# Optimization experiments

Measured on AMD Instinct MI355X. Metric: run time of the kernel, lower is better.

Reference implementation:

```python
import jax, jax.numpy as jnp
import numpy as np

H, KVH, D = 32, 8, 128            # query heads, kv heads, head dim
HIDDEN = H * D                     # 4096
B, S = 32, 2048                    # decode batch, max kv length
THETA = 10000.0
SCALE = D ** -0.5


def setup_inputs() -> dict:
    key = jax.random.key(0)
    ks = jax.random.split(key, 6)
    return {
        "hidden_states": jax.random.normal(ks[0], (B, HIDDEN), jnp.float32),
        "w_qkv": jax.random.normal(ks[1], ((H + 2 * KVH) * D, HIDDEN), jnp.float32) * (HIDDEN ** -0.5),
        "w_o": jax.random.normal(ks[2], (HIDDEN, HIDDEN), jnp.float32) * (HIDDEN ** -0.5),
        "k_cache": jax.random.normal(ks[3], (B, S, KVH, D), jnp.float32),
        "v_cache": jax.random.normal(ks[4], (B, S, KVH, D), jnp.float32),
        "positions": jax.random.randint(ks[5], (B,), 0, S, jnp.int32),
    }


def _rope(x, positions):
    # x: [B, nheads, D], neox-style rotary over full head dim
    half = D // 2
    inv_freq = 1.0 / (THETA ** (jnp.arange(0, half, dtype=jnp.float32) / half))
    freqs = positions.astype(jnp.float32)[:, None] * inv_freq[None, :]   # [B, half]
    cos = jnp.cos(freqs)[:, None, :]
    sin = jnp.sin(freqs)[:, None, :]
    x1, x2 = x[..., :half], x[..., half:]
    return jnp.concatenate([x1 * cos - x2 * sin, x2 * cos + x1 * sin], axis=-1)


def reference(hidden_states, w_qkv, w_o, k_cache, v_cache, positions):
    G = H // KVH  # query heads per kv head
    qkv = hidden_states @ w_qkv.T                      # [B, (H+2*KVH)*D]
    q, k, v = jnp.split(qkv, [H * D, (H + KVH) * D], axis=-1)
    q = _rope(q.reshape(B, H, D), positions)           # [B, H, D]
    k = _rope(k.reshape(B, KVH, D), positions)         # [B, KVH, D]
    v = v.reshape(B, KVH, D)

    # write current token's k/v into the cache at its position (paged-cache write)
    slot = (jnp.arange(S)[None, :] == positions[:, None])[:, :, None, None]  # [B,S,1,1]
    keys = jnp.where(slot, k[:, None], k_cache)        # [B, S, KVH, D]
    vals = jnp.where(slot, v[:, None], v_cache)

    qg = q.reshape(B, KVH, G, D)
    scores = jnp.einsum("bkgd,bskd->bkgs", qg, keys) * SCALE   # [B, KVH, G, S]
    valid = (jnp.arange(S)[None, :] <= positions[:, None])[:, None, None, :]
    scores = jnp.where(valid, scores, -jnp.inf)
    probs = jax.nn.softmax(scores, axis=-1)
    attn = jnp.einsum("bkgs,bskd->bkgd", probs, vals).reshape(B, H * D)
    return attn @ w_o.T                                # [B, HIDDEN]
```

## Files before the change

### kernel.cpp

```cpp
#include <hip/hip_runtime.h>
#include <hip/hip_bf16.h>

#define NH   32
#define NKVH 8
#define NG   4
#define DD   128
#define HID  4096
#define NQKV 6144
#define NB   32
#define SS   2048
#define SCALE 0.08838834764831845f
#define CHUNK 256
#define NCHUNK 8

typedef __attribute__((ext_vector_type(4))) float f32x4;
typedef __attribute__((ext_vector_type(8))) short bf16x8;

static __device__ __forceinline__ unsigned short f2bf(float f) {
    __hip_bfloat16 h = __float2bfloat16(f);
    return __builtin_bit_cast(unsigned short, h);
}

__global__ void cvt_hs(const float* __restrict__ in, unsigned short* __restrict__ out) {
    int i = blockIdx.x * 256 + threadIdx.x;
    out[i] = f2bf(in[i]);
}

__global__ __launch_bounds__(256) void gemm32(
    const unsigned short* __restrict__ Abf,
    const float* __restrict__ W,
    float* __restrict__ Out,
    int K, int N) {
    int j0 = blockIdx.x * 16;
    int tid = threadIdx.x;
    int wave = tid >> 6;
    int lane = tid & 63;
    int l16 = lane & 15;
    int kgrp = lane >> 4;
    int Kq = K >> 2;
    int kbeg = wave * Kq, kend = kbeg + Kq;

    f32x4 acc0 = {0.f, 0.f, 0.f, 0.f};
    f32x4 acc1 = {0.f, 0.f, 0.f, 0.f};
    const unsigned short* arow0 = Abf + (size_t)l16 * K;
    const unsigned short* arow1 = Abf + (size_t)(16 + l16) * K;
    const float* wrow = W + (size_t)(j0 + l16) * K;

#pragma unroll 2
    for (int k = kbeg; k < kend; k += 32) {
        int kk = k + kgrp * 8;
        bf16x8 a0 = *(const bf16x8*)(arow0 + kk);
        bf16x8 a1 = *(const bf16x8*)(arow1 + kk);
        f32x4 w0 = *(const f32x4*)(wrow + kk);
        f32x4 w1 = *(const f32x4*)(wrow + kk + 4);
        bf16x8 bw;
        bw[0] = (short)f2bf(w0[0]); bw[1] = (short)f2bf(w0[1]);
        bw[2] = (short)f2bf(w0[2]); bw[3] = (short)f2bf(w0[3]);
        bw[4] = (short)f2bf(w1[0]); bw[5] = (short)f2bf(w1[1]);
        bw[6] = (short)f2bf(w1[2]); bw[7] = (short)f2bf(w1[3]);
        acc0 = __builtin_amdgcn_mfma_f32_16x16x32_bf16(a0, bw, acc0, 0, 0, 0);
        acc1 = __builtin_amdgcn_mfma_f32_16x16x32_bf16(a1, bw, acc1, 0, 0, 0);
    }

    __shared__ f32x4 red[4][2][64];
    red[wave][0][lane] = acc0;
    red[wave][1][lane] = acc1;
    __syncthreads();
    if (wave == 0) {
        for (int t = 0; t < 2; ++t) {
            f32x4 s = red[0][t][lane];
            s += red[1][t][lane];
            s += red[2][t][lane];
            s += red[3][t][lane];
            for (int r = 0; r < 4; ++r)
                Out[(size_t)(t * 16 + kgrp * 4 + r) * N + j0 + l16] = s[r];
        }
    }
}

__global__ void rope_kernel(const float* __restrict__ qkv, const int* __restrict__ positions,
                            float* __restrict__ q_rope, float* __restrict__ k_rope) {
    int idx = blockIdx.x * 256 + threadIdx.x;
    if (idx >= NB * 40 * 64) return;
    int i = idx & 63;
    int head = (idx >> 6) % 40;
    int b = idx / (64 * 40);
    float pos = (float)positions[b];
    float inv = exp2f(-(float)i * 0.20762050593046f);
    float f = pos * inv;
    float s, c;
    sincosf(f, &s, &c);
    const float* src = qkv + (size_t)b * NQKV + head * DD;
    float x1 = src[i], x2 = src[i + 64];
    float o1 = x1 * c - x2 * s;
    float o2 = x2 * c + x1 * s;
    if (head < NH) {
        float* dst = q_rope + ((size_t)b * NH + head) * DD;
        dst[i] = o1; dst[i + 64] = o2;
    } else {
        float* dst = k_rope + ((size_t)b * NKVH + (head - NH)) * DD;
        dst[i] = o1; dst[i + 64] = o2;
    }
}

__global__ __launch_bounds__(256) void attn_partial(
    const float* __restrict__ k_cache, const float* __restrict__ v_cache,
    const float* __restrict__ q_rope, const float* __restrict__ k_rope,
    const float* __restrict__ qkv, const int* __restrict__ positions,
    float* __restrict__ part) {
    int bk = blockIdx.x;
    int c = blockIdx.y;
    int b = bk >> 3, kvh = bk & 7;
    int pos = positions[b];
    int s0 = c * CHUNK;
    float* mypart = part + ((size_t)bk * NCHUNK + c) * 520;
    int tid = threadIdx.x;
    if (s0 > pos) {
        if (tid < 4) { mypart[tid] = -__builtin_inff(); mypart[4 + tid] = 0.f; }
        return;
    }
    int nvalid = min(pos + 1 - s0, CHUNK);

    __shared__ float sc[4][CHUNK];
    __shared__ float mg[4], lg[4];
    __shared__ f32x4 red[8][4][32];

    for (int i = tid; i < 4 * CHUNK; i += 256) ((float*)sc)[i] = -__builtin_inff();
    __syncthreads();

    int wave = tid >> 6, lane = tid & 63, l16 = lane & 15, rsub = lane >> 4;

    float qf[4][8];
    const float* qbase = q_rope + ((size_t)b * NH + kvh * NG) * DD;
#pragma unroll
    for (int g = 0; g < 4; ++g)
#pragma unroll
        for (int e = 0; e < 8; ++e)
            qf[g][e] = qbase[g * DD + l16 * 8 + e];

    for (int it = 0; it < CHUNK / 16; ++it) {
        int row = it * 16 + wave * 4 + rsub;
        if (row >= nvalid) continue;
        int s = s0 + row;
        const float* krow = (s == pos)
            ? (k_rope + ((size_t)b * NKVH + kvh) * DD)
            : (k_cache + (((size_t)b * SS + s) * NKVH + kvh) * DD);
        f32x4 k0 = *(const f32x4*)(krow + l16 * 8);
        f32x4 k1 = *(const f32x4*)(krow + l16 * 8 + 4);
        float dots[4];
#pragma unroll
        for (int g = 0; g < 4; ++g) {
            dots[g] = qf[g][0] * k0[0] + qf[g][1] * k0[1] + qf[g][2] * k0[2] + qf[g][3] * k0[3]
                    + qf[g][4] * k1[0] + qf[g][5] * k1[1] + qf[g][6] * k1[2] + qf[g][7] * k1[3];
        }
#pragma unroll
        for (int m = 1; m < 16; m <<= 1)
#pragma unroll
            for (int g = 0; g < 4; ++g)
                dots[g] += __shfl_xor(dots[g], m, 64);
        if (l16 == 0)
#pragma unroll
            for (int g = 0; g < 4; ++g) sc[g][row] = dots[g] * SCALE;
    }
    __syncthreads();

    {
        int g = wave;
        float v0 = sc[g][lane], v1 = sc[g][lane + 64], v2 = sc[g][lane + 128], v3 = sc[g][lane + 192];
        float m = fmaxf(fmaxf(v0, v1), fmaxf(v2, v3));
#pragma unroll
        for (int msk = 1; msk < 64; msk <<= 1) m = fmaxf(m, __shfl_xor(m, msk, 64));
        float p0 = expf(v0 - m), p1 = expf(v1 - m), p2 = expf(v2 - m), p3 = expf(v3 - m);
        float l = p0 + p1 + p2 + p3;
#pragma unroll
        for (int msk = 1; msk < 64; msk <<= 1) l += __shfl_xor(l, msk, 64);
        sc[g][lane] = p0; sc[g][lane + 64] = p1; sc[g][lane + 128] = p2; sc[g][lane + 192] = p3;
        if (lane == 0) { mg[g] = m; lg[g] = l; }
    }
    __syncthreads();

    int sid = tid >> 5, l32 = tid & 31;
    f32x4 acc[4] = {{0.f,0.f,0.f,0.f},{0.f,0.f,0.f,0.f},{0.f,0.f,0.f,0.f},{0.f,0.f,0.f,0.f}};
    for (int row = sid; row < nvalid; row += 8) {
        int s = s0 + row;
        const float* vrow = (s == pos)
            ? (qkv + (size_t)b * NQKV + (NH + NKVH) * DD + kvh * DD)
            : (v_cache + (((size_t)b * SS + s) * NKVH + kvh) * DD);
        f32x4 v4 = *(const f32x4*)(vrow + l32 * 4);
#pragma unroll
        for (int g = 0; g < 4; ++g)
            acc[g] += sc[g][row] * v4;
    }
#pragma unroll
    for (int g = 0; g < 4; ++g) red[sid][g][l32] = acc[g];
    __syncthreads();

    if (tid < 128) {
        int g = tid >> 5, l = tid & 31;
        f32x4 s = red[0][g][l];
#pragma unroll
        for (int w = 1; w < 8; ++w) s += red[w][g][l];
        *(f32x4*)(mypart + 8 + g * DD + l * 4) = s;
        if (l == 0) { mypart[g] = mg[g]; mypart[4 + g] = lg[g]; }
    }
}

__global__ __launch_bounds__(128) void attn_combine(
    const float* __restrict__ part, unsigned short* __restrict__ attn_bf) {
    int bk = blockIdx.x;
    int b = bk >> 3, kvh = bk & 7;
    const float* p0 = part + (size_t)bk * NCHUNK * 520;
    int tid = threadIdx.x;
    int g = tid >> 5, l32 = tid & 31;

    float M = -__builtin_inff();
#pragma unroll
    for (int c = 0; c < NCHUNK; ++c) {
        float lcv = p0[c * 520 + 4 + g];
        float mcv = p0[c * 520 + g];
        if (lcv > 0.f && mcv > M) M = mcv;
    }
    float L = 0.f;
    f32x4 acc = {0.f, 0.f, 0.f, 0.f};
#pragma unroll
    for (int c = 0; c < NCHUNK; ++c) {
        float lcv = p0[c * 520 + 4 + g];
        float mcv = p0[c * 520 + g];
        if (lcv > 0.f) {
            float wgt = expf(mcv - M);
            L += lcv * wgt;
            f32x4 a = *(const f32x4*)(p0 + c * 520 + 8 + g * DD + l32 * 4);
            acc += wgt * a;
        }
    }
    float inv = 1.0f / L;
    unsigned short* o = attn_bf + (((size_t)b * NH) + kvh * NG + g) * DD + l32 * 4;
#pragma unroll
    for (int r = 0; r < 4; ++r) o[r] = f2bf(acc[r] * inv);
}

extern "C" void kernel_launch(void* const* d_in, const int* in_sizes, int n_in,
                              void* d_out, int out_size, void* d_ws, size_t ws_size,
                              hipStream_t stream) {
    const float* hs      = (const float*)d_in[0];
    const float* w_qkv   = (const float*)d_in[1];
    const float* w_o     = (const float*)d_in[2];
    const float* k_cache = (const float*)d_in[3];
    const float* v_cache = (const float*)d_in[4];
    const int*   positions = (const int*)d_in[5];
    float* out = (float*)d_out;

    char* ws = (char*)d_ws;
    unsigned short* hs_bf  = (unsigned short*)(ws);
    float* qkv             = (float*)(ws + 262144);
    float* q_rope          = (float*)(ws + 1048576);
    float* k_rope          = (float*)(ws + 1572864);
    float* part            = (float*)(ws + 1703936);
    unsigned short* attn_bf = (unsigned short*)(ws + 5963776);

    hipLaunchKernelGGL(cvt_hs, dim3(512), dim3(256), 0, stream, hs, hs_bf);
    hipLaunchKernelGGL(gemm32, dim3(NQKV / 16), dim3(256), 0, stream, hs_bf, w_qkv, qkv, HID, NQKV);
    hipLaunchKernelGGL(rope_kernel, dim3(320), dim3(256), 0, stream, qkv, positions, q_rope, k_rope);
    hipLaunchKernelGGL(attn_partial, dim3(NB * NKVH, NCHUNK), dim3(256), 0, stream,
                       k_cache, v_cache, q_rope, k_rope, qkv, positions, part);
    hipLaunchKernelGGL(attn_combine, dim3(NB * NKVH), dim3(128), 0, stream, part, attn_bf);
    hipLaunchKernelGGL(gemm32, dim3(HID / 16), dim3(256), 0, stream, attn_bf, w_o, out, HID, HID);
}
```

Before: 135.9 us.

## Split-K both projection GEMMs and halve attention chunk size for more parallelism

Both projection GEMMs now split the K dimension across extra grid blocks and write partial sums: 2 slices for QKV and 4 for the output projection. For QKV, the partial-sum reduction is fused into the RoPE kernel, which also writes the current V row to its own buffer. A new small kernel sums the output-projection partials. The attention split-KV chunk shrinks from 256 to 128 (16 chunks), with the softmax code adjusted to match. The aim is to fill more CUs in these memory-bound, under-occupied kernels, at the cost of extra partial-buffer traffic, an extra launch and a larger combine step.

```diff
diff --git a/kernel.cpp b/kernel.cpp
--- a/kernel.cpp
+++ b/kernel.cpp
@@ -10,8 +10,8 @@
 #define NB   32
 #define SS   2048
 #define SCALE 0.08838834764831845f
-#define CHUNK 256
-#define NCHUNK 8
+#define CHUNK 128
+#define NCHUNK 16
 
 typedef __attribute__((ext_vector_type(4))) float f32x4;
 typedef __attribute__((ext_vector_type(8))) short bf16x8;
@@ -26,19 +26,23 @@
     out[i] = f2bf(in[i]);
 }
 
-__global__ __launch_bounds__(256) void gemm32(
+template<int SPLIT>
+__global__ __launch_bounds__(256) void gemm32_s(
     const unsigned short* __restrict__ Abf,
     const float* __restrict__ W,
-    float* __restrict__ Out,
+    float* __restrict__ Part,
     int K, int N) {
     int j0 = blockIdx.x * 16;
+    int ks = blockIdx.y;
     int tid = threadIdx.x;
     int wave = tid >> 6;
     int lane = tid & 63;
     int l16 = lane & 15;
     int kgrp = lane >> 4;
-    int Kq = K >> 2;
-    int kbeg = wave * Kq, kend = kbeg + Kq;
+    int Kslice = K / SPLIT;
+    int Kq = Kslice >> 2;
+    int kbeg = ks * Kslice + wave * Kq;
+    int kend = kbeg + Kq;
 
     f32x4 acc0 = {0.f, 0.f, 0.f, 0.f};
     f32x4 acc1 = {0.f, 0.f, 0.f, 0.f};
@@ -73,40 +77,49 @@
             s += red[2][t][lane];
             s += red[3][t][lane];
             for (int r = 0; r < 4; ++r)
-                Out[(size_t)(t * 16 + kgrp * 4 + r) * N + j0 + l16] = s[r];
-        }
-    }
-}
-
-__global__ void rope_kernel(const float* __restrict__ qkv, const int* __restrict__ positions,
-                            float* __restrict__ q_rope, float* __restrict__ k_rope) {
+                Part[((size_t)ks * 32 + t * 16 + kgrp * 4 + r) * N + j0 + l16] = s[r];
+        }
+    }
+}
+
+__global__ __launch_bounds__(256) void reduce_rope(
+    const float* __restrict__ part, const int* __restrict__ positions,
+    float* __restrict__ q_rope, float* __restrict__ k_rope, float* __restrict__ vbuf) {
     int idx = blockIdx.x * 256 + threadIdx.x;
-    if (idx >= NB * 40 * 64) return;
-    int i = idx & 63;
-    int head = (idx >> 6) % 40;
-    int b = idx / (64 * 40);
-    float pos = (float)positions[b];
-    float inv = exp2f(-(float)i * 0.20762050593046f);
-    float f = pos * inv;
-    float s, c;
-    sincosf(f, &s, &c);
-    const float* src = qkv + (size_t)b * NQKV + head * DD;
-    float x1 = src[i], x2 = src[i + 64];
-    float o1 = x1 * c - x2 * s;
-    float o2 = x2 * c + x1 * s;
-    if (head < NH) {
-        float* dst = q_rope + ((size_t)b * NH + head) * DD;
-        dst[i] = o1; dst[i + 64] = o2;
-    } else {
-        float* dst = k_rope + ((size_t)b * NKVH + (head - NH)) * DD;
-        dst[i] = o1; dst[i + 64] = o2;
+    const int NROPE = NB * 40 * 64;
+    const int NV = NB * NKVH * DD;
+    if (idx < NROPE) {
+        int i = idx & 63;
+        int head = (idx >> 6) % 40;
+        int b = idx / (64 * 40);
+        size_t base = (size_t)b * NQKV + head * DD;
+        float x1 = part[base + i] + part[(size_t)32 * NQKV + base + i];
+        float x2 = part[base + i + 64] + part[(size_t)32 * NQKV + base + i + 64];
+        float pos = (float)positions[b];
+        float inv = exp2f(-(float)i * 0.20762050593046f);
+        float f = pos * inv;
+        float s, c;
+        sincosf(f, &s, &c);
+        float o1 = x1 * c - x2 * s;
+        float o2 = x2 * c + x1 * s;
+        if (head < NH) {
+            float* dst = q_rope + ((size_t)b * NH + head) * DD;
+            dst[i] = o1; dst[i + 64] = o2;
+        } else {
+            float* dst = k_rope + ((size_t)b * NKVH + (head - NH)) * DD;
+            dst[i] = o1; dst[i + 64] = o2;
+        }
+    } else if (idx < NROPE + NV) {
+        int j = idx - NROPE;
+        size_t base = (size_t)(j >> 10) * NQKV + (NH + NKVH) * DD + (j & 1023);
+        vbuf[j] = part[base] + part[(size_t)32 * NQKV + base];
     }
 }
 
 __global__ __launch_bounds__(256) void attn_partial(
     const float* __restrict__ k_cache, const float* __restrict__ v_cache,
     const float* __restrict__ q_rope, const float* __restrict__ k_rope,
-    const float* __restrict__ qkv, const int* __restrict__ positions,
+    const float* __restrict__ vbuf, const int* __restrict__ positions,
     float* __restrict__ part) {
     int bk = blockIdx.x;
     int c = blockIdx.y;
@@ -166,15 +179,15 @@
 
     {
         int g = wave;
-        float v0 = sc[g][lane], v1 = sc[g][lane + 64], v2 = sc[g][lane + 128], v3 = sc[g][lane + 192];
-        float m = fmaxf(fmaxf(v0, v1), fmaxf(v2, v3));
+        float v0 = sc[g][lane], v1 = sc[g][lane + 64];
+        float m = fmaxf(v0, v1);
 #pragma unroll
         for (int msk = 1; msk < 64; msk <<= 1) m = fmaxf(m, __shfl_xor(m, msk, 64));
-        float p0 = expf(v0 - m), p1 = expf(v1 - m), p2 = expf(v2 - m), p3 = expf(v3 - m);
-        float l = p0 + p1 + p2 + p3;
+        float p0 = expf(v0 - m), p1 = expf(v1 - m);
+        float l = p0 + p1;
 #pragma unroll
         for (int msk = 1; msk < 64; msk <<= 1) l += __shfl_xor(l, msk, 64);
-        sc[g][lane] = p0; sc[g][lane + 64] = p1; sc[g][lane + 128] = p2; sc[g][lane + 192] = p3;
+        sc[g][lane] = p0; sc[g][lane + 64] = p1;
         if (lane == 0) { mg[g] = m; lg[g] = l; }
     }
     __syncthreads();
@@ -184,7 +197,7 @@
     for (int row = sid; row < nvalid; row += 8) {
         int s = s0 + row;
         const float* vrow = (s == pos)
-            ? (qkv + (size_t)b * NQKV + (NH + NKVH) * DD + kvh * DD)
+            ? (vbuf + ((size_t)b * NKVH + kvh) * DD)
             : (v_cache + (((size_t)b * SS + s) * NKVH + kvh) * DD);
         f32x4 v4 = *(const f32x4*)(vrow + l32 * 4);
 #pragma unroll
@@ -237,6 +250,17 @@
     unsigned short* o = attn_bf + (((size_t)b * NH) + kvh * NG + g) * DD + l32 * 4;
 #pragma unroll
     for (int r = 0; r < 4; ++r) o[r] = f2bf(acc[r] * inv);
+}
+
+__global__ __launch_bounds__(256) void reduce_o(const float* __restrict__ part,
+                                                float* __restrict__ out) {
+    int idx = blockIdx.x * 256 + threadIdx.x;
+    const f32x4* p = (const f32x4*)part;
+    f32x4 s = p[idx];
+    s += p[idx + 32768];
+    s += p[idx + 65536];
+    s += p[idx + 98304];
+    ((f32x4*)out)[idx] = s;
 }
 
 extern "C" void kernel_launch(void* const* d_in, const int* in_sizes, int n_in,
@@ -251,18 +275,24 @@
     float* out = (float*)d_out;
 
     char* ws = (char*)d_ws;
-    unsigned short* hs_bf  = (unsigned short*)(ws);
-    float* qkv             = (float*)(ws + 262144);
-    float* q_rope          = (float*)(ws + 1048576);
-    float* k_rope          = (float*)(ws + 1572864);
-    float* part            = (float*)(ws + 1703936);
-    unsigned short* attn_bf = (unsigned short*)(ws + 5963776);
+    unsigned short* hs_bf   = (unsigned short*)(ws);
+    float* qkv_part         = (float*)(ws + 262144);
+    float* q_rope           = (float*)(ws + 1835008);
+    float* k_rope           = (float*)(ws + 2359296);
+    float* vbuf             = (float*)(ws + 2490368);
+    float* part             = (float*)(ws + 2621440);
+    unsigned short* attn_bf = (unsigned short*)(ws + 11141120);
+    float* o_part           = (float*)(ws + 11403264);
 
     hipLaunchKernelGGL(cvt_hs, dim3(512), dim3(256), 0, stream, hs, hs_bf);
-    hipLaunchKernelGGL(gemm32, dim3(NQKV / 16), dim3(256), 0, stream, hs_bf, w_qkv, qkv, HID, NQKV);
-    hipLaunchKernelGGL(rope_kernel, dim3(320), dim3(256), 0, stream, qkv, positions, q_rope, k_rope);
+    hipLaunchKernelGGL((gemm32_s<2>), dim3(NQKV / 16, 2), dim3(256), 0, stream,
+                       hs_bf, w_qkv, qkv_part, HID, NQKV);
+    hipLaunchKernelGGL(reduce_rope, dim3(448), dim3(256), 0, stream,
+                       qkv_part, positions, q_rope, k_rope, vbuf);
     hipLaunchKernelGGL(attn_partial, dim3(NB * NKVH, NCHUNK), dim3(256), 0, stream,
-                       k_cache, v_cache, q_rope, k_rope, qkv, positions, part);
+                       k_cache, v_cache, q_rope, k_rope, vbuf, positions, part);
     hipLaunchKernelGGL(attn_combine, dim3(NB * NKVH), dim3(128), 0, stream, part, attn_bf);
-    hipLaunchKernelGGL(gemm32, dim3(HID / 16), dim3(256), 0, stream, attn_bf, w_o, out, HID, HID);
-}
+    hipLaunchKernelGGL((gemm32_s<4>), dim3(HID / 16, 4), dim3(256), 0, stream,
+                       attn_bf, w_o, o_part, HID, HID);
+    hipLaunchKernelGGL(reduce_o, dim3(128), dim3(256), 0, stream, o_part, out);
+}
```

New measurement: 130.9 us. -3.6%, faster.
